# Kernel optimization log

Hardware: AMD Instinct MI355X
Metric: run time of the kernel (lower is better)

The kernel has to match this reference:

```python
import jax, jax.numpy as jnp
import numpy as np

WS = 8
NH = 16
EPS = 1e-5

# relative position index (static, same as the torch buffer)
def _rel_index(ws):
    coords = np.stack(np.meshgrid(np.arange(ws), np.arange(ws), indexing='ij'))  # 2,ws,ws
    flat = coords.reshape(2, -1)
    rel = flat[:, :, None] - flat[:, None, :]
    rel = rel.transpose(1, 2, 0).copy()
    rel[..., 0] += ws - 1
    rel[..., 1] += ws - 1
    rel[..., 0] *= 2 * ws - 1
    return rel.sum(-1)  # (ws*ws, ws*ws)

REL_IDX = jnp.asarray(_rel_index(WS))

def conv2d(x, w, dilation=1, pad=None, groups=1):
    k = w.shape[-1]
    if pad is None:
        pad = (dilation * (k - 1)) // 2
    return jax.lax.conv_general_dilated(
        x, w, (1, 1), ((pad, pad), (pad, pad)), rhs_dilation=(dilation, dilation),
        dimension_numbers=('NCHW', 'OIHW', 'NCHW'), feature_group_count=groups)

def bn(x, p):
    g, b, m, v = p[0], p[1], p[2], p[3]
    inv = g / jnp.sqrt(v + EPS)
    return x * inv[:, None, None] + (b - m * inv)[:, None, None]

def avgpool(x, kh, kw, ph, pw):
    # torch AvgPool2d with count_include_pad=True: zero-pad then divide by kernel size
    s = jax.lax.reduce_window(x, 0.0, jax.lax.add, (1, 1, kh, kw), (1, 1, 1, 1),
                              ((0, 0), (0, 0), (ph, ph), (pw, pw)))
    return s / (kh * kw)

def _fwd(x, w_pre, bn_pre, w_l1, bn_l1, w_l2, bn_l2, w_l3, bn_l3, w_qkv, rpb, w_dw, w_pw, bn_proj):
    B, C, H, W = x.shape
    # local conv branch (chunk 256 -> 86,86,84 with dilations 1,2,3)
    local = bn(conv2d(x, w_pre), bn_pre)
    l1 = bn(conv2d(local[:, :86], w_l1, dilation=1), bn_l1)
    l2 = bn(conv2d(local[:, 86:172], w_l2, dilation=2), bn_l2)
    l3 = bn(conv2d(local[:, 172:], w_l3, dilation=3), bn_l3)
    local = jnp.concatenate([l1, l2, l3], axis=1)
    # pad to window multiple (reflect); static shapes so Python branch is fine
    ph, pw = (-H) % WS, (-W) % WS
    if ph or pw:
        x = jnp.pad(x, ((0, 0), (0, 0), (0, ph), (0, pw)), mode='reflect')
    Hp, Wp = H + ph, W + pw
    hh, ww = Hp // WS, Wp // WS
    d = C // NH
    qkv = conv2d(x, w_qkv)  # (B, 3C, Hp, Wp)
    qkv = qkv.reshape(B, 3, NH, d, hh, WS, ww, WS)
    qkv = qkv.transpose(1, 0, 4, 6, 2, 5, 7, 3).reshape(3, B * hh * ww, NH, WS * WS, d)
    q, k, v = qkv[0], qkv[1], qkv[2]
    dots = jnp.einsum('whid,whjd->whij', q, k) * (d ** -0.5)
    bias = rpb[REL_IDX.reshape(-1)].reshape(WS * WS, WS * WS, NH).transpose(2, 0, 1)
    attn = jax.nn.softmax(dots + bias[None], axis=-1)
    out = jnp.einsum('whij,whjd->whid', attn, v)
    out = out.reshape(B, hh, ww, NH, WS, WS, d).transpose(0, 3, 6, 1, 4, 2, 5).reshape(B, C, Hp, Wp)
    out = out[:, :, :H, :W]
    ax = avgpool(jnp.pad(out, ((0, 0), (0, 0), (0, 1), (0, 0)), mode='reflect'), WS, 1, WS // 2 - 1, 0)
    ay = avgpool(jnp.pad(out, ((0, 0), (0, 0), (0, 0), (0, 1)), mode='reflect'), 1, WS, 0, WS // 2 - 1)
    out = ax + ay + local
    out = jnp.pad(out, ((0, 0), (0, 0), (0, 1), (0, 1)), mode='reflect')
    out = conv2d(out, w_dw, pad=3, groups=C)       # depthwise 8x8
    out = bn(conv2d(out, w_pw), bn_proj)           # pointwise + BN
    return out[:, :, :H, :W]

def setup_inputs() -> dict:
    key = jax.random.key(0)
    ks = jax.random.split(key, 16)
    def w(k, shape, s=0.05):
        return jax.random.normal(k, shape, dtype=jnp.float32) * s
    def bnp(k, c):
        p = jax.random.uniform(k, (4, c), dtype=jnp.float32)
        return p.at[3].add(0.5)  # keep var positive and away from 0
    return {
        'x': jax.random.normal(ks[0], (8, 256, 128, 128), dtype=jnp.float32),
        'w_pre': w(ks[1], (256, 256, 1, 1)), 'bn_pre': bnp(ks[2], 256),
        'w_l1': w(ks[3], (86, 86, 3, 3)), 'bn_l1': bnp(ks[4], 86),
        'w_l2': w(ks[5], (86, 86, 3, 3)), 'bn_l2': bnp(ks[6], 86),
        'w_l3': w(ks[7], (84, 84, 3, 3)), 'bn_l3': bnp(ks[8], 84),
        'w_qkv': w(ks[9], (768, 256, 1, 1)),
        'rpb': w(ks[10], (225, 16), 0.02),
        'w_dw': w(ks[11], (256, 1, 8, 8)),
        'w_pw': w(ks[12], (256, 256, 1, 1)),
        'bn_proj': bnp(ks[13], 256),
    }

def reference(x, w_pre, bn_pre, w_l1, bn_l1, w_l2, bn_l2, w_l3, bn_l3, w_qkv, rpb, w_dw, w_pw, bn_proj):
    return _fwd(x, w_pre, bn_pre, w_l1, bn_l1, w_l2, bn_l2, w_l3, bn_l3, w_qkv, rpb, w_dw, w_pw, bn_proj)
```

## Files before the change

kernel.cpp:

```cpp
#include <hip/hip_runtime.h>
#include <hip/hip_bf16.h>
#include <cstdint>
#include <cstddef>

namespace {

constexpr int HW = 16384;

typedef short vec8s __attribute__((ext_vector_type(8)));
typedef float f32x4 __attribute__((ext_vector_type(4)));

__device__ __forceinline__ float u2f(uint32_t u){ union { uint32_t u; float f; } v; v.u = u; return v.f; }
__device__ __forceinline__ uint32_t f2u(float f){ union { float f; uint32_t u; } v; v.f = f; return v.u; }
__device__ __forceinline__ uint16_t f2bf(float f){
  uint32_t u = f2u(f);
  u += 0x7fffu + ((u >> 16) & 1u);
  return (uint16_t)(u >> 16);
}
__device__ __forceinline__ void unpack2(uint32_t w, float& lo, float& hi){
  lo = u2f(w << 16);
  hi = u2f(w & 0xffff0000u);
}

__global__ __launch_bounds__(256) void k_w2bf(
    const float* __restrict__ src, uint16_t* __restrict__ dst, int n)
{
  int i = (blockIdx.x * 256 + threadIdx.x) * 8;
  if (i + 8 <= n) {
    float4 a = *(const float4*)(src + i);
    float4 b = *(const float4*)(src + i + 4);
    uint4 pk;
    pk.x = (uint32_t)f2bf(a.x) | ((uint32_t)f2bf(a.y) << 16);
    pk.y = (uint32_t)f2bf(a.z) | ((uint32_t)f2bf(a.w) << 16);
    pk.z = (uint32_t)f2bf(b.x) | ((uint32_t)f2bf(b.y) << 16);
    pk.w = (uint32_t)f2bf(b.z) | ((uint32_t)f2bf(b.w) << 16);
    *(uint4*)(dst + i) = pk;
  }
}

__global__ __launch_bounds__(256) void k_cast(
    const float* __restrict__ x, uint16_t* __restrict__ xT)
{
  __shared__ float sF[64][129];
  const int t = threadIdx.x;
  const int b = blockIdx.x >> 7;
  const int y = blockIdx.x & 127;
  const size_t rowoff = (size_t)y * 128;
  for (int cc = 0; cc < 4; ++cc) {
    const int cic0 = cc * 64;
    #pragma unroll
    for (int k = 0; k < 8; ++k) {
      int e = t + k * 256;
      int ci = e >> 5;
      int pxq = (e & 31) * 4;
      float4 v = *(const float4*)(x + (size_t)(b * 256 + cic0 + ci) * HW + rowoff + pxq);
      sF[ci][pxq] = v.x; sF[ci][pxq+1] = v.y; sF[ci][pxq+2] = v.z; sF[ci][pxq+3] = v.w;
    }
    __syncthreads();
    {
      int px = t >> 1, h = t & 1;
      __align__(16) uint16_t tmp[32];
      #pragma unroll
      for (int j = 0; j < 32; ++j) tmp[j] = f2bf(sF[h * 32 + j][px]);
      uint16_t* dst = xT + ((size_t)b * HW + rowoff + px) * 256 + cic0 + h * 32;
      *(uint4*)(dst)      = *(uint4*)&tmp[0];
      *(uint4*)(dst + 8)  = *(uint4*)&tmp[8];
      *(uint4*)(dst + 16) = *(uint4*)&tmp[16];
      *(uint4*)(dst + 24) = *(uint4*)&tmp[24];
    }
    __syncthreads();
  }
}

template<int OUT_MODE, int NCO>
__global__ __launch_bounds__(256) void k_gemm_v2(
    const uint16_t* __restrict__ xT, const uint16_t* __restrict__ wbf,
    const float* __restrict__ bnp, int M,
    uint16_t* __restrict__ outb, float* __restrict__ outf)
{
  __shared__ __align__(16) uint16_t sX[128][260];
  __shared__ __align__(16) uint16_t sW[128][36];
  const int t = threadIdx.x;
  const int b    = blockIdx.x >> 7;
  const int tile = blockIdx.x & 127;
  const int l = t & 63, w = t >> 6;
  const int l15 = l & 15, koct = l >> 4;
  const int wc = w >> 1, wp = w & 1;

  {
    const int spx = t >> 1, sh = t & 1;
    int gpx;
    if constexpr (OUT_MODE == 3) {
      int win = tile * 2 + (spx >> 6);
      int p = spx & 63;
      gpx = ((win >> 4) * 8 + (p >> 3)) * 128 + (win & 15) * 8 + (p & 7);
    } else {
      gpx = tile * 128 + spx;
    }
    const uint16_t* src = xT + ((size_t)b * HW + gpx) * 256 + sh * 128;
    uint16_t* dst = &sX[spx][sh * 128];
    #pragma unroll
    for (int i = 0; i < 16; ++i)
      *(uint4*)(dst + i * 8) = *(const uint4*)(src + i * 8);
  }

  const int swc = t >> 1, swh = t & 1;
  uint4 wr0, wr1;
  {
    const uint16_t* p = wbf + (size_t)swc * 256 + swh * 16;
    wr0 = *(const uint4*)(p);
    wr1 = *(const uint4*)(p + 8);
  }
  __syncthreads();

  for (int cc = 0; cc < NCO; ++cc) {
    f32x4 acc[4][4];
    #pragma unroll
    for (int cf = 0; cf < 4; ++cf)
      #pragma unroll
      for (int pf = 0; pf < 4; ++pf) acc[cf][pf] = (f32x4){0.f,0.f,0.f,0.f};

    for (int kc = 0; kc < 8; ++kc) {
      if (cc | kc) __syncthreads();
      {
        uint16_t* dst = &sW[swc][swh * 16];
        *(uint4*)(dst)     = wr0;
        *(uint4*)(dst + 8) = wr1;
      }
      {
        int nkc = kc + 1, ncc = cc;
        if (nkc == 8) { nkc = 0; ncc = cc + 1; }
        if (ncc < NCO) {
          const uint16_t* p = wbf + (size_t)(ncc * 128 + swc) * 256 + nkc * 32 + swh * 16;
          wr0 = *(const uint4*)(p);
          wr1 = *(const uint4*)(p + 8);
        }
      }
      __syncthreads();
      vec8s bf[4];
      #pragma unroll
      for (int pf = 0; pf < 4; ++pf)
        bf[pf] = *(const vec8s*)&sX[wp * 64 + pf * 16 + l15][kc * 32 + koct * 8];
      #pragma unroll
      for (int cf = 0; cf < 4; ++cf) {
        vec8s af = *(const vec8s*)&sW[wc * 64 + cf * 16 + l15][koct * 8];
        #pragma unroll
        for (int pf = 0; pf < 4; ++pf)
          acc[cf][pf] = __builtin_amdgcn_mfma_f32_16x16x32_bf16(af, bf[pf], acc[cf][pf], 0, 0, 0);
      }
    }

    #pragma unroll
    for (int cf = 0; cf < 4; ++cf) {
      const int cbase = cc * 128 + wc * 64 + cf * 16 + koct * 4;
      float scv[4], shv[4];
      #pragma unroll
      for (int r = 0; r < 4; ++r) {
        scv[r] = 1.f; shv[r] = 0.f;
        if constexpr (OUT_MODE == 0 || OUT_MODE == 2) {
          int c = cbase + r;
          float g = bnp[c], be = bnp[M + c], mu = bnp[2 * M + c], va = bnp[3 * M + c];
          scv[r] = g * rsqrtf(va + 1e-5f);
          shv[r] = be - mu * scv[r];
        }
      }
      #pragma unroll
      for (int pf = 0; pf < 4; ++pf) {
        if constexpr (OUT_MODE == 0) {
          int px = tile * 128 + wp * 64 + pf * 16 + l15;
          __align__(8) uint16_t pk[4];
          #pragma unroll
          for (int r = 0; r < 4; ++r)
            pk[r] = f2bf(fmaf(acc[cf][pf][r], scv[r], shv[r]));
          *(uint2*)(outb + ((size_t)b * HW + px) * 256 + cbase) = *(uint2*)pk;
        } else if constexpr (OUT_MODE == 2) {
          int px = tile * 128 + wp * 64 + pf * 16 + l15;
          #pragma unroll
          for (int r = 0; r < 4; ++r)
            outf[(size_t)(b * M + cbase + r) * HW + px] =
                fmaf(acc[cf][pf][r], scv[r], shv[r]);
        } else {
          int win = tile * 2 + wp;
          int p = pf * 16 + l15;
          uint16_t* dstp = outb + ((size_t)(b * 256 + win) * 768 + cbase) * 64 + p;
          #pragma unroll
          for (int r = 0; r < 4; ++r)
            dstp[(size_t)r * 64] = f2bf(acc[cf][pf][r]);
        }
      }
    }
  }
}

template<int DIL, int CG>
__global__ __launch_bounds__(256) void k_dilconv_mfma(
    const uint16_t* __restrict__ preT, const float* __restrict__ wt,
    const float* __restrict__ bnp, float* __restrict__ out,
    int cb, int cb_al)
{
  constexpr int R = 8 + 2 * DIL;
  constexpr int C = 64 + 2 * DIL;
  constexpr int NPOS = R * C;
  constexpr int NIT = (NPOS + 255) / 256;
  __shared__ __align__(16) uint16_t sX[NPOS * 16];
  __shared__ __align__(16) uint16_t sW[10 * 50 * 16];

  const int t = threadIdx.x;
  const int rt    = blockIdx.x >> 1;
  const int ctile = blockIdx.x & 1;
  const int ct2   = blockIdx.y;
  const int b     = blockIdx.z;
  const int y0 = rt * 8, x0 = ctile * 64;
  const int l = t & 63, w = t >> 6;
  const int l15 = l & 15, oct = (l >> 4) & 1, half = l >> 5;
  const int rbase = w * 2;

  f32x4 acc[3][8];
  #pragma unroll
  for (int cf = 0; cf < 3; ++cf)
    #pragma unroll
    for (int q = 0; q < 8; ++q) acc[cf][q] = (f32x4){0.f,0.f,0.f,0.f};

  for (int kc = 0; kc < 6; ++kc) {
    #pragma unroll
    for (int i = 0; i < 3; ++i) {
      int pair = t + i * 256;
      int co = pair >> 4, ci = pair & 15;
      int cog = ct2 * 48 + co;
      int c = cb_al + kc * 16 + ci;
      bool ok = (cog < CG) && (c >= cb) && (c < cb + CG);
      size_t widx = ok ? ((size_t)cog * (size_t)CG + (size_t)(c - cb)) * 9u
                       : (size_t)0;
      const float* wp = wt + widx;
      uint16_t* dst = &sW[co * 16 + ci];
      #pragma unroll
      for (int tap = 0; tap < 9; ++tap)
        dst[tap * 800] = ok ? f2bf(wp[tap]) : (uint16_t)0;
      dst[9 * 800] = 0;
    }
    #pragma unroll
    for (int i = 0; i < NIT; ++i) {
      int p = t + i * 256;
      if (p < NPOS) {
        int row = p / C, col = p % C;
        int gy = y0 + row - DIL, gx = x0 + col - DIL;
        uint4 va = {0,0,0,0}, vb = {0,0,0,0};
        if ((unsigned)gy < 128u && (unsigned)gx < 128u) {
          const uint4* src = (const uint4*)(preT +
              (((size_t)b * HW + gy * 128 + gx) * 256 + cb_al + kc * 16));
          va = src[0]; vb = src[1];
        }
        uint4* dst = (uint4*)&sX[p * 16];
        dst[0] = va; dst[1] = vb;
      }
    }
    __syncthreads();

    #pragma unroll
    for (int s = 0; s < 5; ++s) {
      const int tap0 = 2 * s, tap1 = 2 * s + 1;
      const int dy0 = tap0 / 3, dx0 = tap0 % 3;
      const int dy1 = (tap1 <= 8) ? tap1 / 3 : 2;
      const int dx1 = (tap1 <= 8) ? tap1 % 3 : 2;
      const int dy = half ? dy1 : dy0;
      const int dx = half ? dx1 : dx0;
      const int atap = tap0 + half;
      vec8s a0 = *(const vec8s*)&sW[(atap * 50 + 0  + l15) * 16 + oct * 8];
      vec8s a1 = *(const vec8s*)&sW[(atap * 50 + 16 + l15) * 16 + oct * 8];
      vec8s a2 = *(const vec8s*)&sW[(atap * 50 + 32 + l15) * 16 + oct * 8];
      #pragma unroll
      for (int rs = 0; rs < 2; ++rs) {
        const int rowin = rbase + rs + dy * DIL;
        #pragma unroll
        for (int c4 = 0; c4 < 4; ++c4) {
          const int colin = c4 * 16 + l15 + dx * DIL;
          vec8s bf = *(const vec8s*)&sX[(rowin * C + colin) * 16 + oct * 8];
          acc[0][rs*4+c4] = __builtin_amdgcn_mfma_f32_16x16x32_bf16(a0, bf, acc[0][rs*4+c4], 0, 0, 0);
          acc[1][rs*4+c4] = __builtin_amdgcn_mfma_f32_16x16x32_bf16(a1, bf, acc[1][rs*4+c4], 0, 0, 0);
          acc[2][rs*4+c4] = __builtin_amdgcn_mfma_f32_16x16x32_bf16(a2, bf, acc[2][rs*4+c4], 0, 0, 0);
        }
      }
    }
    __syncthreads();
  }

  const int row4 = (l >> 4);
  #pragma unroll
  for (int cf = 0; cf < 3; ++cf) {
    #pragma unroll
    for (int r = 0; r < 4; ++r) {
      int c_loc = ct2 * 48 + cf * 16 + row4 * 4 + r;
      if (c_loc < CG) {
        int cg = cb + c_loc;
        float g = bnp[c_loc], be = bnp[CG + c_loc];
        float mu = bnp[2 * CG + c_loc], va = bnp[3 * CG + c_loc];
        float scv = g * rsqrtf(va + 1e-5f);
        float shv = be - mu * scv;
        #pragma unroll
        for (int rs = 0; rs < 2; ++rs) {
          int y = y0 + rbase + rs;
          #pragma unroll
          for (int c4 = 0; c4 < 4; ++c4) {
            int x = x0 + c4 * 16 + l15;
            out[(size_t)(b * 256 + cg) * HW + y * 128 + x] =
                fmaf(acc[cf][rs*4+c4][r], scv, shv);
          }
        }
      }
    }
  }
}

__global__ __launch_bounds__(256) void k_attn(
    const uint16_t* __restrict__ qkvW, const float* __restrict__ rpb,
    uint16_t* __restrict__ outp)
{
  __shared__ __align__(16) uint16_t sAll[4][5632];
  const int t = threadIdx.x;
  const int l = t & 63, w = t >> 6;
  const int l15 = l & 15, koct = l >> 4;
  const int b = blockIdx.y;
  const int win = blockIdx.x;
  const int wy = win >> 4, wx = win & 15;
  const int wbase = (wy * 8) * 128 + wx * 8;
  const uint16_t* base = qkvW + (size_t)(b * 256 + win) * 49152;
  uint16_t* swKT = &sAll[w][0];
  uint16_t* swQT = &sAll[w][2560];
  uint16_t* swPT = &sAll[w][0];
  float*    swO  = (float*)&sAll[w][0];
  float*    swB  = (float*)&sAll[w][5120];

  const uint16_t* qg = base + (size_t)(w * 16) * 64;
  const uint16_t* kg = qg + 256 * 64;
  const uint16_t* vg = qg + 512 * 64;
  uint32_t kp[8], qp[8];
  float breg[4];
  #pragma unroll
  for (int m = 0; m < 8; ++m) {
    uint32_t k0 = kg[(2 * m) * 64 + l], k1 = kg[(2 * m + 1) * 64 + l];
    uint32_t q0 = qg[(2 * m) * 64 + l], q1 = qg[(2 * m + 1) * 64 + l];
    kp[m] = k0 | (k1 << 16);
    qp[m] = q0 | (q1 << 16);
  }
  #pragma unroll
  for (int m = 0; m < 4; ++m) {
    int e = l + m * 64;
    breg[m] = (e < 225) ? rpb[e * 16 + w] : 0.f;
  }

  for (int it = 0; it < 4; ++it) {
    const int n = w + it * 4;
    #pragma unroll
    for (int m = 0; m < 4; ++m) {
      int e = l + m * 64;
      if (e < 225) swB[e] = breg[m];
    }
    {
      uint4 z = {0, 0, 0, 0};
      *(uint4*)(swKT + l * 40)      = *(uint4*)&kp[0];
      *(uint4*)(swKT + l * 40 + 8)  = *(uint4*)&kp[4];
      *(uint4*)(swKT + l * 40 + 16) = z;
      *(uint4*)(swKT + l * 40 + 24) = z;
      *(uint4*)(swQT + l * 40)      = *(uint4*)&qp[0];
      *(uint4*)(swQT + l * 40 + 8)  = *(uint4*)&qp[4];
      *(uint4*)(swQT + l * 40 + 16) = z;
      *(uint4*)(swQT + l * 40 + 24) = z;
    }
    vec8s vA0 = *(const vec8s*)(vg + l15 * 64 + koct * 8);
    vec8s vA1 = *(const vec8s*)(vg + l15 * 64 + 32 + koct * 8);
    if (it < 3) {
      const uint16_t* qg2 = qg + 4096;
      const uint16_t* kg2 = kg + 4096;
      #pragma unroll
      for (int m = 0; m < 8; ++m) {
        uint32_t k0 = kg2[(2 * m) * 64 + l], k1 = kg2[(2 * m + 1) * 64 + l];
        uint32_t q0 = qg2[(2 * m) * 64 + l], q1 = qg2[(2 * m + 1) * 64 + l];
        kp[m] = k0 | (k1 << 16);
        qp[m] = q0 | (q1 << 16);
      }
      #pragma unroll
      for (int m = 0; m < 4; ++m) {
        int e = l + m * 64;
        breg[m] = (e < 225) ? rpb[e * 16 + n + 4] : 0.f;
      }
    }
    asm volatile("s_waitcnt lgkmcnt(0)" ::: "memory");
    __builtin_amdgcn_sched_barrier(0);

    vec8s aK[4], bQ[4];
    #pragma unroll
    for (int tt = 0; tt < 4; ++tt) {
      aK[tt] = *(const vec8s*)(swKT + (tt * 16 + l15) * 40 + koct * 8);
      bQ[tt] = *(const vec8s*)(swQT + (tt * 16 + l15) * 40 + koct * 8);
    }
    f32x4 accS[4][4];
    #pragma unroll
    for (int ti = 0; ti < 4; ++ti)
      #pragma unroll
      for (int tj = 0; tj < 4; ++tj)
        accS[ti][tj] = __builtin_amdgcn_mfma_f32_16x16x32_bf16(
            aK[tj], bQ[ti], (f32x4){0.f, 0.f, 0.f, 0.f}, 0, 0, 0);

    float p[4][16], sinv[4];
    #pragma unroll
    for (int ti = 0; ti < 4; ++ti) {
      const int i = ti * 16 + l15;
      const int irow = i >> 3, icol = i & 7;
      #pragma unroll
      for (int tj = 0; tj < 4; ++tj) {
        #pragma unroll
        for (int r = 0; r < 4; ++r) {
          int j = tj * 16 + koct * 4 + r;
          int rel = (irow - (j >> 3) + 7) * 15 + (icol - (j & 7) + 7);
          p[ti][tj * 4 + r] = fmaf(accS[ti][tj][r], 0.25f, swB[rel]);
        }
      }
      float mx = p[ti][0];
      #pragma unroll
      for (int u = 1; u < 16; ++u) mx = fmaxf(mx, p[ti][u]);
      mx = fmaxf(mx, __shfl_xor(mx, 16));
      mx = fmaxf(mx, __shfl_xor(mx, 32));
      float s = 0.f;
      #pragma unroll
      for (int u = 0; u < 16; ++u) { p[ti][u] = __expf(p[ti][u] - mx); s += p[ti][u]; }
      s += __shfl_xor(s, 16);
      s += __shfl_xor(s, 32);
      sinv[ti] = 1.f / s;
    }

    #pragma unroll
    for (int ti = 0; ti < 4; ++ti) {
      uint16_t* rowp = swPT + (ti * 16 + l15) * 68 + koct * 4;
      #pragma unroll
      for (int tj = 0; tj < 4; ++tj) {
        uint32_t u0 = (uint32_t)f2bf(p[ti][tj * 4 + 0]) | ((uint32_t)f2bf(p[ti][tj * 4 + 1]) << 16);
        uint32_t u1 = (uint32_t)f2bf(p[ti][tj * 4 + 2]) | ((uint32_t)f2bf(p[ti][tj * 4 + 3]) << 16);
        *(uint32_t*)(rowp + tj * 16)     = u0;
        *(uint32_t*)(rowp + tj * 16 + 2) = u1;
      }
    }
    asm volatile("s_waitcnt lgkmcnt(0)" ::: "memory");
    __builtin_amdgcn_sched_barrier(0);

    f32x4 accO[4];
    #pragma unroll
    for (int ii = 0; ii < 4; ++ii) accO[ii] = (f32x4){0.f, 0.f, 0.f, 0.f};
    #pragma unroll
    for (int ks = 0; ks < 2; ++ks) {
      vec8s aV = ks ? vA1 : vA0;
      #pragma unroll
      for (int ii = 0; ii < 4; ++ii) {
        vec8s bP;
        const uint16_t* src = swPT + (ii * 16 + l15) * 68 + ks * 32 + koct * 8;
        *(uint2*)&bP       = *(const uint2*)(src);
        *((uint2*)&bP + 1) = *(const uint2*)(src + 4);
        accO[ii] = __builtin_amdgcn_mfma_f32_16x16x32_bf16(aV, bP, accO[ii], 0, 0, 0);
      }
    }
    asm volatile("s_waitcnt lgkmcnt(0)" ::: "memory");
    __builtin_amdgcn_sched_barrier(0);

    #pragma unroll
    for (int ii = 0; ii < 4; ++ii) {
      #pragma unroll
      for (int r = 0; r < 4; ++r) {
        int dd = koct * 4 + r;
        swO[dd * 76 + ii * 16 + l15] = accO[ii][r] * sinv[ii];
      }
    }
    asm volatile("s_waitcnt lgkmcnt(0)" ::: "memory");
    __builtin_amdgcn_sched_barrier(0);
    #pragma unroll
    for (int e2 = 0; e2 < 2; ++e2) {
      int e = l + e2 * 64;
      int dd = e >> 3, row = e & 7;
      const float* orow = swO + dd * 76 + row * 8;
      float4 a = *(const float4*)(orow);
      float4 c = *(const float4*)(orow + 4);
      uint4 pk;
      pk.x = (uint32_t)f2bf(a.x) | ((uint32_t)f2bf(a.y) << 16);
      pk.y = (uint32_t)f2bf(a.z) | ((uint32_t)f2bf(a.w) << 16);
      pk.z = (uint32_t)f2bf(c.x) | ((uint32_t)f2bf(c.y) << 16);
      pk.w = (uint32_t)f2bf(c.z) | ((uint32_t)f2bf(c.w) << 16);
      *(uint4*)(outp + (size_t)(b * 256 + n * 16 + dd) * HW + wbase + row * 128) = pk;
    }
    asm volatile("s_waitcnt lgkmcnt(0)" ::: "memory");
    __builtin_amdgcn_sched_barrier(0);
    qg += 4096; kg += 4096; vg += 4096;
  }
}

__global__ __launch_bounds__(256) void k_pool(
    const uint16_t* __restrict__ attnb, float* __restrict__ loc)
{
  __shared__ __align__(16) float sP[71][136];
  const int t = threadIdx.x;
  const int plane = blockIdx.x >> 1;
  const int h0 = (blockIdx.x & 1) * 64;
  const size_t pbase = (size_t)plane * HW;
  #pragma unroll
  for (int k = 0; k < 5; ++k) {
    int idx = t + k * 256;
    if (idx < 71 * 16) {
      int lr = idx >> 4, m = idx & 15;
      int g = h0 - 3 + lr;
      float f[8] = {0.f,0.f,0.f,0.f,0.f,0.f,0.f,0.f};
      if (g >= 0 && g <= 127) {
        uint4 v4 = *(const uint4*)(attnb + pbase + (size_t)g * 128 + m * 8);
        unpack2(v4.x, f[0], f[1]); unpack2(v4.y, f[2], f[3]);
        unpack2(v4.z, f[4], f[5]); unpack2(v4.w, f[6], f[7]);
      }
      float* dst = &sP[lr][4 + m * 8];
      *(float4*)dst       = (float4){f[0], f[1], f[2], f[3]};
      *(float4*)(dst + 4) = (float4){f[4], f[5], f[6], f[7]};
    }
  }
  #pragma unroll
  for (int k = 0; k < 3; ++k) {
    int idx = t + k * 256;
    if (idx < 71 * 8) {
      int lr = idx >> 3, e = idx & 7;
      int c = (e < 4) ? e : (128 + e);
      sP[lr][c] = 0.f;
    }
  }
  __syncthreads();

  const int q  = t & 31;
  const int r0 = (t >> 5) * 8;
  const int w0 = q * 4;
  float4 av = {0.f, 0.f, 0.f, 0.f};
  #pragma unroll
  for (int o = 0; o < 8; ++o) {
    float4 v = *(const float4*)&sP[r0 + o][4 + w0];
    av.x += v.x; av.y += v.y; av.z += v.z; av.w += v.w;
  }
  #pragma unroll
  for (int rr = 0; rr < 8; ++rr) {
    const int lh = r0 + rr;
    const int h = h0 + lh;
    float4 a = av;
    if (h >= 124) {
      float4 cfix = *(const float4*)&sP[126 - 64 + 3][4 + w0];
      a.x += cfix.x; a.y += cfix.y; a.z += cfix.z; a.w += cfix.w;
    }
    float4 hv0 = *(const float4*)&sP[lh + 3][w0];
    float4 hv1 = *(const float4*)&sP[lh + 3][w0 + 4];
    float4 hv2 = *(const float4*)&sP[lh + 3][w0 + 8];
    float s0 = hv0.y + hv0.z + hv0.w + hv1.x + hv1.y + hv1.z + hv1.w + hv2.x;
    float s1 = s0 - hv0.y + hv2.y;
    float s2 = s1 - hv0.z + hv2.z;
    float s3 = s2 - hv0.w + hv2.w;
    if (q == 31) {
      float cfix = sP[lh + 3][130];
      s0 += cfix; s1 += cfix; s2 += cfix; s3 += cfix;
    }
    const size_t gi = pbase + (size_t)h * 128 + w0;
    float4 lv = *(const float4*)(loc + gi);
    float4 o4;
    o4.x = fmaf(a.x + s0, 0.125f, lv.x);
    o4.y = fmaf(a.y + s1, 0.125f, lv.y);
    o4.z = fmaf(a.z + s2, 0.125f, lv.z);
    o4.w = fmaf(a.w + s3, 0.125f, lv.w);
    *(float4*)(loc + gi) = o4;
    if (rr < 7) {
      float4 vm = *(const float4*)&sP[lh][4 + w0];
      float4 vp = *(const float4*)&sP[lh + 8][4 + w0];
      av.x += vp.x - vm.x; av.y += vp.y - vm.y;
      av.z += vp.z - vm.z; av.w += vp.w - vm.w;
    }
  }
}

__global__ __launch_bounds__(256) void k_dw(
    const float* __restrict__ comb, const float* __restrict__ wdw,
    float* __restrict__ out)
{
  __shared__ __align__(16) float sZ[71][136];
  __shared__ float sWd[64];
  const int t = threadIdx.x;
  const int plane = blockIdx.x >> 1;
  const int cch = plane & 255;
  const int h0 = (blockIdx.x & 1) * 64;
  const size_t pbase = (size_t)plane * HW;
  if (t < 64) sWd[t] = wdw[cch * 64 + t];
  #pragma unroll
  for (int k = 0; k < 5; ++k) {
    int idx = t + k * 256;
    if (idx < 71 * 16) {
      int lr = idx >> 4, m = idx & 15;
      int g = h0 - 3 + lr;
      float4 a = {0.f,0.f,0.f,0.f}, c = {0.f,0.f,0.f,0.f};
      if (g >= 0 && g <= 128) {
        int gr = (g == 128) ? 126 : g;
        const float* src = comb + pbase + (size_t)gr * 128 + m * 8;
        a = *(const float4*)(src);
        c = *(const float4*)(src + 4);
      }
      float* dst = &sZ[lr][4 + m * 8];
      *(float4*)dst       = a;
      *(float4*)(dst + 4) = c;
    }
  }
  if (t < 71) {
    int lr = t;
    int g = h0 - 3 + lr;
    float rv = 0.f;
    if (g >= 0 && g <= 128) {
      int gr = (g == 128) ? 126 : g;
      rv = comb[pbase + (size_t)gr * 128 + 126];
    }
    *(float4*)&sZ[lr][0] = (float4){0.f, 0.f, 0.f, 0.f};
    sZ[lr][132] = rv;
    sZ[lr][133] = 0.f; sZ[lr][134] = 0.f; sZ[lr][135] = 0.f;
  }
  __syncthreads();

  float wt[8][8];
  #pragma unroll
  for (int i = 0; i < 8; ++i) {
    *(float4*)&wt[i][0] = *(const float4*)&sWd[i * 8];
    *(float4*)&wt[i][4] = *(const float4*)&sWd[i * 8 + 4];
  }

  const int q  = t & 31;
  const int rg = t >> 5;
  const int w0 = q * 4;
  f32x4 acc[8];
  #pragma unroll
  for (int rr = 0; rr < 8; ++rr) acc[rr] = (f32x4){0.f,0.f,0.f,0.f};

  #pragma unroll
  for (int v = 0; v < 15; ++v) {
    const int lr = rg * 8 + v;
    float win[12];
    *(float4*)&win[0] = *(const float4*)&sZ[lr][w0];
    *(float4*)&win[4] = *(const float4*)&sZ[lr][w0 + 4];
    *(float4*)&win[8] = *(const float4*)&sZ[lr][w0 + 8];
    #pragma unroll
    for (int rr = 0; rr < 8; ++rr) {
      const int i = v - rr;
      if (i >= 0 && i < 8) {
        #pragma unroll
        for (int c = 0; c < 4; ++c) {
          float s = acc[rr][c];
          #pragma unroll
          for (int j = 0; j < 8; ++j)
            s = fmaf(wt[i][j], win[c + j + 1], s);
          acc[rr][c] = s;
        }
      }
    }
  }
  #pragma unroll
  for (int rr = 0; rr < 8; ++rr) {
    int h = h0 + rg * 8 + rr;
    float* dst = out + pbase + (size_t)h * 128 + w0;
    *(float4*)dst = (float4){acc[rr][0], acc[rr][1], acc[rr][2], acc[rr][3]};
  }
}

}

extern "C" void kernel_launch(void* const* d_in, const int* in_sizes, int n_in,
                              void* d_out, int out_size, void* d_ws, size_t ws_size,
                              hipStream_t stream)
{
  const float* x      = (const float*)d_in[0];
  const float* w_pre  = (const float*)d_in[1];
  const float* bn_pre = (const float*)d_in[2];
  const float* w_l1   = (const float*)d_in[3];
  const float* bn_l1  = (const float*)d_in[4];
  const float* w_l2   = (const float*)d_in[5];
  const float* bn_l2  = (const float*)d_in[6];
  const float* w_l3   = (const float*)d_in[7];
  const float* bn_l3  = (const float*)d_in[8];
  const float* w_qkv  = (const float*)d_in[9];
  const float* rpb    = (const float*)d_in[10];
  const float* w_dw   = (const float*)d_in[11];
  const float* w_pw   = (const float*)d_in[12];
  const float* bn_pj  = (const float*)d_in[13];
  float* out = (float*)d_out;

  char* base = (char*)d_ws;
  uint16_t* xT    = (uint16_t*)base;
  uint16_t* preT  = (uint16_t*)(base + (size_t)67108864);
  float*    bufB  = (float*)(base + (size_t)134217728);
  uint16_t* bufQ  = (uint16_t*)(base + (size_t)268435456);
  uint16_t* attnO = preT;
  float*    bufDw = (float*)bufQ;
  uint16_t* dwT   = xT;
  uint16_t* wpre_bf = (uint16_t*)out;
  uint16_t* wqkv_bf = wpre_bf + 65536;
  uint16_t* wpw_bf  = preT;

  dim3 blk(256);
  k_w2bf<<<dim3(32),  blk, 0, stream>>>(w_pre, wpre_bf, 65536);
  k_w2bf<<<dim3(96),  blk, 0, stream>>>(w_qkv, wqkv_bf, 196608);
  k_cast<<<dim3(1024), blk, 0, stream>>>(x, xT);
  k_gemm_v2<0, 2><<<dim3(1024), blk, 0, stream>>>(xT, wpre_bf, bn_pre, 256, preT, nullptr);
  k_dilconv_mfma<1, 86><<<dim3(32, 2, 8), blk, 0, stream>>>(preT, w_l1, bn_l1, bufB, 0, 0);
  k_dilconv_mfma<2, 86><<<dim3(32, 2, 8), blk, 0, stream>>>(preT, w_l2, bn_l2, bufB, 86, 80);
  k_dilconv_mfma<3, 84><<<dim3(32, 2, 8), blk, 0, stream>>>(preT, w_l3, bn_l3, bufB, 172, 160);
  k_gemm_v2<3, 6><<<dim3(1024), blk, 0, stream>>>(xT, wqkv_bf, nullptr, 768, bufQ, nullptr);
  k_attn<<<dim3(256, 8), blk, 0, stream>>>(bufQ, rpb, attnO);
  k_pool<<<dim3(4096), blk, 0, stream>>>(attnO, bufB);
  k_w2bf<<<dim3(32), blk, 0, stream>>>(w_pw, wpw_bf, 65536);
  k_dw<<<dim3(4096), blk, 0, stream>>>(bufB, w_dw, bufDw);
  k_cast<<<dim3(1024), blk, 0, stream>>>(bufDw, dwT);
  k_gemm_v2<2, 2><<<dim3(1024), blk, 0, stream>>>(dwT, wpw_bf, bn_pj, 256, nullptr, out);

  (void)in_sizes; (void)n_in; (void)out_size; (void)ws_size;
}
```

Measured before the change: 720.2 us.

## Fuse fp32-to-bf16 cast into GEMM loads and merge pre and qkv projections

The separate transpose/cast kernels are removed, and the GEMM now loads fp32 NCHW input directly, converting to bf16 into shared memory. The pre-conv 1x1 and qkv 1x1 projections are merged into one GEMM over a concatenated 1024-row weight, with window-ordered pixel tiles. The first 256 output channels are written with BN to preT at scattered pixel positions, and the rest go to the qkv window buffer. This removes the intermediate xT/dwT round trips and one full read of the input, at the cost of strided scalar shared-memory stores during staging.

Result: faster. 642.7 us, median of 2 (-10.8%).

```diff
diff --git a/kernel.cpp b/kernel.cpp
--- a/kernel.cpp
+++ b/kernel.cpp
@@ -38,45 +38,12 @@
   }
 }
 
-__global__ __launch_bounds__(256) void k_cast(
-    const float* __restrict__ x, uint16_t* __restrict__ xT)
-{
-  __shared__ float sF[64][129];
-  const int t = threadIdx.x;
-  const int b = blockIdx.x >> 7;
-  const int y = blockIdx.x & 127;
-  const size_t rowoff = (size_t)y * 128;
-  for (int cc = 0; cc < 4; ++cc) {
-    const int cic0 = cc * 64;
-    #pragma unroll
-    for (int k = 0; k < 8; ++k) {
-      int e = t + k * 256;
-      int ci = e >> 5;
-      int pxq = (e & 31) * 4;
-      float4 v = *(const float4*)(x + (size_t)(b * 256 + cic0 + ci) * HW + rowoff + pxq);
-      sF[ci][pxq] = v.x; sF[ci][pxq+1] = v.y; sF[ci][pxq+2] = v.z; sF[ci][pxq+3] = v.w;
-    }
-    __syncthreads();
-    {
-      int px = t >> 1, h = t & 1;
-      __align__(16) uint16_t tmp[32];
-      #pragma unroll
-      for (int j = 0; j < 32; ++j) tmp[j] = f2bf(sF[h * 32 + j][px]);
-      uint16_t* dst = xT + ((size_t)b * HW + rowoff + px) * 256 + cic0 + h * 32;
-      *(uint4*)(dst)      = *(uint4*)&tmp[0];
-      *(uint4*)(dst + 8)  = *(uint4*)&tmp[8];
-      *(uint4*)(dst + 16) = *(uint4*)&tmp[16];
-      *(uint4*)(dst + 24) = *(uint4*)&tmp[24];
-    }
-    __syncthreads();
-  }
-}
-
-template<int OUT_MODE, int NCO>
-__global__ __launch_bounds__(256) void k_gemm_v2(
-    const uint16_t* __restrict__ xT, const uint16_t* __restrict__ wbf,
-    const float* __restrict__ bnp, int M,
-    uint16_t* __restrict__ outb, float* __restrict__ outf)
+template<int OUT_MODE, int NCO, bool WINM>
+__global__ __launch_bounds__(256) void k_gemm_v4(
+    const float* __restrict__ xf, const uint16_t* __restrict__ wbf,
+    const float* __restrict__ bnp,
+    uint16_t* __restrict__ outbPre, uint16_t* __restrict__ outbQkv,
+    float* __restrict__ outf)
 {
   __shared__ __align__(16) uint16_t sX[128][260];
   __shared__ __align__(16) uint16_t sW[128][36];
@@ -88,20 +55,26 @@
   const int wc = w >> 1, wp = w & 1;
 
   {
-    const int spx = t >> 1, sh = t & 1;
+    const int cig = t >> 5;
+    const int pq  = (t & 31) * 4;
     int gpx;
-    if constexpr (OUT_MODE == 3) {
-      int win = tile * 2 + (spx >> 6);
-      int p = spx & 63;
+    if constexpr (WINM) {
+      int win = tile * 2 + (pq >> 6);
+      int p = pq & 63;
       gpx = ((win >> 4) * 8 + (p >> 3)) * 128 + (win & 15) * 8 + (p & 7);
     } else {
-      gpx = tile * 128 + spx;
-    }
-    const uint16_t* src = xT + ((size_t)b * HW + gpx) * 256 + sh * 128;
-    uint16_t* dst = &sX[spx][sh * 128];
-    #pragma unroll
-    for (int i = 0; i < 16; ++i)
-      *(uint4*)(dst + i * 8) = *(const uint4*)(src + i * 8);
+      gpx = tile * 128 + pq;
+    }
+    const float* srcb = xf + (size_t)b * 256 * HW + gpx;
+    #pragma unroll
+    for (int cb8 = 0; cb8 < 32; ++cb8) {
+      int ci = cb8 * 8 + cig;
+      float4 v = *(const float4*)(srcb + (size_t)ci * HW);
+      sX[pq][ci]     = f2bf(v.x);
+      sX[pq + 1][ci] = f2bf(v.y);
+      sX[pq + 2][ci] = f2bf(v.z);
+      sX[pq + 3][ci] = f2bf(v.w);
+    }
   }
 
   const int swc = t >> 1, swh = t & 1;
@@ -153,39 +126,56 @@
     #pragma unroll
     for (int cf = 0; cf < 4; ++cf) {
       const int cbase = cc * 128 + wc * 64 + cf * 16 + koct * 4;
-      float scv[4], shv[4];
-      #pragma unroll
-      for (int r = 0; r < 4; ++r) {
-        scv[r] = 1.f; shv[r] = 0.f;
-        if constexpr (OUT_MODE == 0 || OUT_MODE == 2) {
+      if constexpr (OUT_MODE == 2) {
+        float scv[4], shv[4];
+        #pragma unroll
+        for (int r = 0; r < 4; ++r) {
           int c = cbase + r;
-          float g = bnp[c], be = bnp[M + c], mu = bnp[2 * M + c], va = bnp[3 * M + c];
+          float g = bnp[c], be = bnp[256 + c], mu = bnp[512 + c], va = bnp[768 + c];
           scv[r] = g * rsqrtf(va + 1e-5f);
           shv[r] = be - mu * scv[r];
         }
-      }
-      #pragma unroll
-      for (int pf = 0; pf < 4; ++pf) {
-        if constexpr (OUT_MODE == 0) {
-          int px = tile * 128 + wp * 64 + pf * 16 + l15;
-          __align__(8) uint16_t pk[4];
-          #pragma unroll
-          for (int r = 0; r < 4; ++r)
-            pk[r] = f2bf(fmaf(acc[cf][pf][r], scv[r], shv[r]));
-          *(uint2*)(outb + ((size_t)b * HW + px) * 256 + cbase) = *(uint2*)pk;
-        } else if constexpr (OUT_MODE == 2) {
+        #pragma unroll
+        for (int pf = 0; pf < 4; ++pf) {
           int px = tile * 128 + wp * 64 + pf * 16 + l15;
           #pragma unroll
           for (int r = 0; r < 4; ++r)
-            outf[(size_t)(b * M + cbase + r) * HW + px] =
+            outf[(size_t)(b * 256 + cbase + r) * HW + px] =
                 fmaf(acc[cf][pf][r], scv[r], shv[r]);
+        }
+      } else {
+        if (cc < 2) {
+          float scv[4], shv[4];
+          #pragma unroll
+          for (int r = 0; r < 4; ++r) {
+            int c = cbase + r;
+            float g = bnp[c], be = bnp[256 + c], mu = bnp[512 + c], va = bnp[768 + c];
+            scv[r] = g * rsqrtf(va + 1e-5f);
+            shv[r] = be - mu * scv[r];
+          }
+          #pragma unroll
+          for (int pf = 0; pf < 4; ++pf) {
+            int e = wp * 64 + pf * 16 + l15;
+            int win = tile * 2 + (e >> 6);
+            int p = e & 63;
+            int gpx = ((win >> 4) * 8 + (p >> 3)) * 128 + (win & 15) * 8 + (p & 7);
+            __align__(8) uint16_t pk[4];
+            #pragma unroll
+            for (int r = 0; r < 4; ++r)
+              pk[r] = f2bf(fmaf(acc[cf][pf][r], scv[r], shv[r]));
+            *(uint2*)(outbPre + ((size_t)b * HW + gpx) * 256 + cbase) = *(uint2*)pk;
+          }
         } else {
-          int win = tile * 2 + wp;
-          int p = pf * 16 + l15;
-          uint16_t* dstp = outb + ((size_t)(b * 256 + win) * 768 + cbase) * 64 + p;
+          const int c0 = cbase - 256;
           #pragma unroll
-          for (int r = 0; r < 4; ++r)
-            dstp[(size_t)r * 64] = f2bf(acc[cf][pf][r]);
+          for (int pf = 0; pf < 4; ++pf) {
+            int win = tile * 2 + wp;
+            int p = pf * 16 + l15;
+            uint16_t* dstp = outbQkv + ((size_t)(b * 256 + win) * 768 + c0) * 64 + p;
+            #pragma unroll
+            for (int r = 0; r < 4; ++r)
+              dstp[(size_t)r * 64] = f2bf(acc[cf][pf][r]);
+          }
         }
       }
     }
@@ -683,32 +673,28 @@
   float* out = (float*)d_out;
 
   char* base = (char*)d_ws;
-  uint16_t* xT    = (uint16_t*)base;
   uint16_t* preT  = (uint16_t*)(base + (size_t)67108864);
   float*    bufB  = (float*)(base + (size_t)134217728);
   uint16_t* bufQ  = (uint16_t*)(base + (size_t)268435456);
   uint16_t* attnO = preT;
   float*    bufDw = (float*)bufQ;
-  uint16_t* dwT   = xT;
-  uint16_t* wpre_bf = (uint16_t*)out;
-  uint16_t* wqkv_bf = wpre_bf + 65536;
-  uint16_t* wpw_bf  = preT;
+  uint16_t* wcomb_bf = (uint16_t*)out;
+  uint16_t* wpw_bf   = preT;
 
   dim3 blk(256);
-  k_w2bf<<<dim3(32),  blk, 0, stream>>>(w_pre, wpre_bf, 65536);
-  k_w2bf<<<dim3(96),  blk, 0, stream>>>(w_qkv, wqkv_bf, 196608);
-  k_cast<<<dim3(1024), blk, 0, stream>>>(x, xT);
-  k_gemm_v2<0, 2><<<dim3(1024), blk, 0, stream>>>(xT, wpre_bf, bn_pre, 256, preT, nullptr);
+  k_w2bf<<<dim3(32),  blk, 0, stream>>>(w_pre, wcomb_bf, 65536);
+  k_w2bf<<<dim3(96),  blk, 0, stream>>>(w_qkv, wcomb_bf + 65536, 196608);
+  k_gemm_v4<4, 8, true><<<dim3(1024), blk, 0, stream>>>(
+      x, wcomb_bf, bn_pre, preT, bufQ, nullptr);
   k_dilconv_mfma<1, 86><<<dim3(32, 2, 8), blk, 0, stream>>>(preT, w_l1, bn_l1, bufB, 0, 0);
   k_dilconv_mfma<2, 86><<<dim3(32, 2, 8), blk, 0, stream>>>(preT, w_l2, bn_l2, bufB, 86, 80);
   k_dilconv_mfma<3, 84><<<dim3(32, 2, 8), blk, 0, stream>>>(preT, w_l3, bn_l3, bufB, 172, 160);
-  k_gemm_v2<3, 6><<<dim3(1024), blk, 0, stream>>>(xT, wqkv_bf, nullptr, 768, bufQ, nullptr);
   k_attn<<<dim3(256, 8), blk, 0, stream>>>(bufQ, rpb, attnO);
   k_pool<<<dim3(4096), blk, 0, stream>>>(attnO, bufB);
   k_w2bf<<<dim3(32), blk, 0, stream>>>(w_pw, wpw_bf, 65536);
   k_dw<<<dim3(4096), blk, 0, stream>>>(bufB, w_dw, bufDw);
-  k_cast<<<dim3(1024), blk, 0, stream>>>(bufDw, dwT);
-  k_gemm_v2<2, 2><<<dim3(1024), blk, 0, stream>>>(dwT, wpw_bf, bn_pj, 256, nullptr, out);
+  k_gemm_v4<2, 2, false><<<dim3(1024), blk, 0, stream>>>(
+      bufDw, wpw_bf, bn_pj, nullptr, nullptr, out);
 
   (void)in_sizes; (void)n_in; (void)out_size; (void)ws_size;
 }
```
